# Performance work log

Measured on AMD Instinct MI355X. Metric: run time of the kernel, lower is better.

The kernel has to match this reference:

```python
import jax, jax.numpy as jnp
import numpy as np

EPS = 1e-6

def normalize(a):
    # L1 row-normalization over the last dim (works for [b,f,n,n] and [b,n,n])
    return a / (jnp.sum(jnp.abs(a), axis=-1, keepdims=True) + EPS)

def setup_inputs() -> dict:
    key = jax.random.key(0)
    ks = jax.random.split(key, 10)
    B, NC, F_, NE, R = 32, 62, 256, 512, 16
    s = 0.05
    return {
        "x": jax.random.normal(ks[0], (B, NC, F_), dtype=jnp.float32),
        "p": jax.random.normal(ks[1], (NC, NC), dtype=jnp.float32) * s,
        "bias": jnp.zeros((NC, F_), dtype=jnp.float32),
        "q_mat": jax.random.normal(ks[2], (F_, F_), dtype=jnp.float32) * s,
        "theta": jax.random.normal(ks[3], (F_, NC * F_), dtype=jnp.float32) * s,
        "codebook": jax.random.normal(ks[4], (NE, F_), dtype=jnp.float32) * s,
        "se_w1": jax.random.normal(ks[5], (F_, F_ // R), dtype=jnp.float32) * s,
        "se_b1": jnp.zeros((F_ // R,), dtype=jnp.float32),
        "se_w2": jax.random.normal(ks[6], (F_ // R, F_), dtype=jnp.float32) * s,
        "se_b2": jnp.zeros((F_,), dtype=jnp.float32),
    }

def reference(x, p, bias, q_mat, theta, codebook, se_w1, se_b1, se_w2, se_b2):
    elu = jax.nn.elu
    commitment = 0.25
    # o = p @ x + bias : [b, nc, f]
    o = jnp.einsum('ij,bjd->bid', p, x) + bias
    # g = ELU(o @ q @ theta) : [b, nc, nc*f]
    g = elu((o @ q_mat) @ theta)
    b, nc = g.shape[0], g.shape[1]
    adj = g.reshape(b, nc, nc, -1).transpose(0, 3, 1, 2)  # [b, f, nc, nc]
    adj = normalize(adj)
    # ---- VQ codebook quantization ----
    d = codebook.shape[1]
    z = adj.transpose(0, 2, 3, 1).reshape(-1, d)  # [b*nc*nc, d]
    dist = (jnp.sum(z * z, axis=-1, keepdims=True)
            - 2.0 * z @ codebook.T
            + jnp.sum(codebook * codebook, axis=-1))  # [N, num_embedding]
    idx = jnp.argmin(dist, axis=-1)
    zq = codebook[idx]
    e_loss = jnp.mean((jax.lax.stop_gradient(zq) - z) ** 2)
    q_loss = jnp.mean((zq - jax.lax.stop_gradient(z)) ** 2)
    vq_loss = q_loss + commitment * e_loss
    zq_st = z + jax.lax.stop_gradient(zq - z)  # straight-through
    counts = jnp.zeros((codebook.shape[0],), dtype=z.dtype).at[idx].add(1.0)
    probs = counts / idx.shape[0]
    usage = jnp.exp(-jnp.sum(probs * jnp.log(probs + 1e-10)))  # perplexity
    adj_recon = zq_st.reshape(b, nc, nc, d).transpose(0, 3, 1, 2)  # [b, f, nc, nc]
    # ---- SE block + residual ----
    s = jnp.mean(adj_recon, axis=(2, 3))  # squeeze: [b, f]
    s = jax.nn.sigmoid(jax.nn.relu(s @ se_w1 + se_b1) @ se_w2 + se_b2)
    adj_recon = elu(adj_recon * s[:, :, None, None] + adj_recon)
    # reduce over feature channels, ELU, normalize : [b, nc, nc]
    adj_recon = normalize(elu(jnp.sum(adj_recon, axis=1)))
    return (vq_loss, adj_recon, usage, codebook)
```

## Files before the change

kernel.cpp:

```cpp
#include <hip/hip_runtime.h>
#include <math.h>

#define B_   32
#define NCq  62
#define F_   256
#define NE   512
#define M_   (B_*NCq)
#define NCOL (NCq*F_)
#define NZ   (M_*NCq)
#define EPSF 1e-6f

typedef unsigned short ushort_t;
typedef unsigned int uint_t;
typedef _Float16 h8_t __attribute__((ext_vector_type(8)));
typedef float f4_t __attribute__((ext_vector_type(4)));

__device__ __forceinline__ float eluf(float x){ return x > 0.0f ? x : expm1f(x); }

__device__ __forceinline__ int sw64(int row, int piece){
    return row*64 + ((piece ^ (row&7))*8);
}
__device__ __forceinline__ void gl_lds(const _Float16* g, _Float16* l){
    __builtin_amdgcn_global_load_lds((const __attribute__((address_space(1))) void*)g,
                                     (__attribute__((address_space(3))) void*)l, 16, 0, 0);
}

__global__ __launch_bounds__(256) void k_split_th(const float* __restrict__ TH,
                                                  _Float16* __restrict__ THf){
    __shared__ float tile[32][33];
    int n0 = blockIdx.x * 32, k0 = blockIdx.y * 32;
    int tid = threadIdx.x;
    int cc = tid & 31, rr = tid >> 5;
    #pragma unroll
    for(int p=0;p<4;p++){
        int kk = rr + p*8;
        tile[kk][cc] = TH[(size_t)(k0+kk)*NCOL + n0 + cc];
    }
    __syncthreads();
    #pragma unroll
    for(int p=0;p<4;p++){
        int nn = rr + p*8;
        THf[(size_t)(n0+nn)*F_ + k0 + cc] = (_Float16)tile[cc][nn];
    }
}

__global__ __launch_bounds__(256) void k_prep(const float* __restrict__ cb,
                                              _Float16* __restrict__ CBf,
                                              float* __restrict__ cnorm, float* __restrict__ out_cb){
    int e = blockIdx.x; int d = threadIdx.x;
    float v = cb[e*F_ + d];
    out_cb[e*F_ + d] = v;
    CBf[e*F_ + d] = (_Float16)v;
    float s = v*v;
    #pragma unroll
    for(int m=32;m;m>>=1) s += __shfl_xor(s, m, 64);
    __shared__ float red[4];
    if((threadIdx.x & 63)==0) red[threadIdx.x>>6] = s;
    __syncthreads();
    if(threadIdx.x==0) cnorm[e] = red[0]+red[1]+red[2]+red[3];
}

__global__ __launch_bounds__(256) void k_ot(const float* __restrict__ x, const float* __restrict__ p,
                                            const float* __restrict__ bias, const float* __restrict__ q,
                                            _Float16* __restrict__ Tf){
    int bi = blockIdx.x; int d = threadIdx.x;
    int b = bi / NCq, i = bi % NCq;
    __shared__ float pr[NCq];
    __shared__ float orow[F_];
    if(d < NCq) pr[d] = p[i*NCq + d];
    __syncthreads();
    float acc = bias[i*F_ + d];
    const float* xb = x + (size_t)b*NCq*F_ + d;
    #pragma unroll 2
    for(int j=0;j<NCq;j++) acc = fmaf(pr[j], xb[j*F_], acc);
    orow[d] = acc;
    __syncthreads();
    float t = 0.f;
    #pragma unroll 4
    for(int k=0;k<F_;k++) t = fmaf(orow[k], q[k*F_ + d], t);
    Tf[bi*F_ + d] = (_Float16)t;
}

__global__ __launch_bounds__(256,2) void k_gemm_g(const _Float16* __restrict__ Tf,
                                                  const _Float16* __restrict__ THf,
                                                  _Float16* __restrict__ Gf){
    __shared__ _Float16 As[128*64], Bs[256*64];
    int tid = threadIdx.x;
    int l = tid & 63, w = tid >> 6;
    int wr = w >> 1, wc = w & 1;
    int m = l & 15, quad = l >> 4;
    int row0 = blockIdx.x * 128, col0 = blockIdx.y * 256;
    int wbase = tid & 192;
    f4_t acc[4][8] = {};
    for(int kc=0; kc<F_; kc+=64){
        #pragma unroll
        for(int p2=0;p2<4;p2++){
            int idx = p2*256 + tid;
            int row = idx >> 3, psw = idx & 7;
            int porig = psw ^ (row&7);
            int rclamp = row0 + row; if(rclamp >= M_) rclamp = M_-1;
            gl_lds(&Tf[(size_t)rclamp*F_ + kc + porig*8], &As[(p2*256 + wbase)*8]);
        }
        #pragma unroll
        for(int p2=0;p2<8;p2++){
            int idx = p2*256 + tid;
            int row = idx >> 3, psw = idx & 7;
            int porig = psw ^ (row&7);
            gl_lds(&THf[(size_t)(col0 + row)*F_ + kc + porig*8], &Bs[(p2*256 + wbase)*8]);
        }
        __syncthreads();
        #pragma unroll
        for(int ks=0;ks<2;ks++){
            h8_t a[4];
            #pragma unroll
            for(int mt=0;mt<4;mt++){
                int row = wr*64 + mt*16 + m;
                a[mt] = *(const h8_t*)&As[sw64(row, ks*4 + quad)];
            }
            #pragma unroll
            for(int nt=0;nt<8;nt++){
                int col = wc*128 + nt*16 + m;
                h8_t b = *(const h8_t*)&Bs[sw64(col, ks*4 + quad)];
                #pragma unroll
                for(int mt=0;mt<4;mt++)
                    acc[mt][nt] = __builtin_amdgcn_mfma_f32_16x16x32_f16(a[mt], b, acc[mt][nt], 0,0,0);
            }
        }
        __syncthreads();
    }
    #pragma unroll
    for(int mt=0;mt<4;mt++){
        #pragma unroll
        for(int nt=0;nt<8;nt++){
            int rowb = row0 + wr*64 + mt*16 + quad*4;
            int colb = col0 + wc*128 + nt*16 + m;
            #pragma unroll
            for(int r=0;r<4;r++){
                int row = rowb + r;
                if(row < M_) Gf[(size_t)row*NCOL + colb] = (_Float16)eluf(acc[mt][nt][r]);
            }
        }
    }
}

__global__ __launch_bounds__(256) void k_den(_Float16* __restrict__ Gf, double* __restrict__ loss_sum){
    int bi = blockIdx.x;
    int tid = threadIdx.x;
    int dg = tid & 31, jg = tid >> 5;
    __shared__ float l1[8][32][8];
    __shared__ float l2[8][32][8];
    __shared__ float invsh[32][8];
    float v[8][8];
    float a1[8] = {}, a2[8] = {};
    size_t base = (size_t)bi*NCOL + dg*8;
    #pragma unroll
    for(int p=0;p<8;p++){
        int j = jg + p*8;
        if(j < NCq){
            h8_t g = *(const h8_t*)&Gf[base + (size_t)j*F_];
            #pragma unroll
            for(int i=0;i<8;i++){
                float t = (float)g[i];
                v[p][i] = t;
                a1[i] += fabsf(t);
                a2[i] = fmaf(t, t, a2[i]);
            }
        }
    }
    #pragma unroll
    for(int i=0;i<8;i++){ l1[jg][dg][i] = a1[i]; l2[jg][dg][i] = a2[i]; }
    __syncthreads();
    if(jg == 0){
        float part = 0.f;
        #pragma unroll
        for(int i=0;i<8;i++){
            float s1 = 0.f, s2 = 0.f;
            #pragma unroll
            for(int q2=0;q2<8;q2++){ s1 += l1[q2][dg][i]; s2 += l2[q2][dg][i]; }
            float inv = 1.0f/(s1 + EPSF);
            invsh[dg][i] = inv;
            part += s2*inv*inv;
        }
        #pragma unroll
        for(int mk=16;mk;mk>>=1) part += __shfl_xor(part, mk, 32);
        if(tid == 0) atomicAdd(loss_sum, (double)part);
    }
    __syncthreads();
    float inv[8];
    #pragma unroll
    for(int i=0;i<8;i++) inv[i] = invsh[dg][i];
    #pragma unroll
    for(int p=0;p<8;p++){
        int j = jg + p*8;
        if(j < NCq){
            h8_t z;
            #pragma unroll
            for(int i=0;i<8;i++) z[i] = (_Float16)(v[p][i]*inv[i]);
            *(h8_t*)&Gf[base + (size_t)j*F_] = z;
        }
    }
}

__global__ __launch_bounds__(256,2) void k_vq(const _Float16* __restrict__ Zf,
                                              const _Float16* __restrict__ CBf,
                                              const float* __restrict__ cnorm,
                                              float* __restrict__ pmin, int* __restrict__ pidx){
    __shared__ _Float16 As[128*64], Bs[256*64];
    int tid = threadIdx.x;
    int l = tid & 63, w = tid >> 6;
    int wr = w >> 1, wc = w & 1;
    int m = l & 15, quad = l >> 4;
    int n_base = blockIdx.x * 128;
    int e0 = blockIdx.y * 256;
    int wbase = tid & 192;
    f4_t acc[4][8] = {};
    for(int kc=0; kc<F_; kc+=64){
        #pragma unroll
        for(int p2=0;p2<4;p2++){
            int idx = p2*256 + tid;
            int row = idx >> 3, psw = idx & 7;
            int porig = psw ^ (row&7);
            gl_lds(&Zf[(size_t)(n_base + row)*F_ + kc + porig*8], &As[(p2*256 + wbase)*8]);
        }
        #pragma unroll
        for(int p2=0;p2<8;p2++){
            int idx = p2*256 + tid;
            int row = idx >> 3, psw = idx & 7;
            int porig = psw ^ (row&7);
            gl_lds(&CBf[(size_t)(e0 + row)*F_ + kc + porig*8], &Bs[(p2*256 + wbase)*8]);
        }
        __syncthreads();
        #pragma unroll
        for(int ks=0;ks<2;ks++){
            h8_t a[4];
            #pragma unroll
            for(int mt=0;mt<4;mt++){
                int row = wr*64 + mt*16 + m;
                a[mt] = *(const h8_t*)&As[sw64(row, ks*4 + quad)];
            }
            #pragma unroll
            for(int nt=0;nt<8;nt++){
                int col = wc*128 + nt*16 + m;
                h8_t b = *(const h8_t*)&Bs[sw64(col, ks*4 + quad)];
                #pragma unroll
                for(int mt=0;mt<4;mt++)
                    acc[mt][nt] = __builtin_amdgcn_mfma_f32_16x16x32_f16(a[mt], b, acc[mt][nt], 0,0,0);
            }
        }
        __syncthreads();
    }
    #pragma unroll
    for(int mt=0;mt<4;mt++){
        float bv[4]; int bix[4];
        #pragma unroll
        for(int r=0;r<4;r++){ bv[r] = 3.4e38f; bix[r] = 0; }
        #pragma unroll
        for(int nt=0;nt<8;nt++){
            int e = e0 + wc*128 + nt*16 + m;
            float cn = cnorm[e];
            #pragma unroll
            for(int r=0;r<4;r++){
                float vv = cn - 2.0f*acc[mt][nt][r];
                if(vv < bv[r]){ bv[r] = vv; bix[r] = e; }
            }
        }
        #pragma unroll
        for(int r=0;r<4;r++){
            float vv = bv[r]; int ix = bix[r];
            #pragma unroll
            for(int mk=8;mk;mk>>=1){
                float ov = __shfl_xor(vv, mk, 64);
                int   oi = __shfl_xor(ix, mk, 64);
                if(ov < vv || (ov == vv && oi < ix)){ vv = ov; ix = oi; }
            }
            if(m == 0){
                int n = n_base + wr*64 + mt*16 + quad*4 + r;
                int slot = blockIdx.y*2 + wc;
                pmin[n*4 + slot] = vv;
                pidx[n*4 + slot] = ix;
            }
        }
    }
}

__global__ __launch_bounds__(1024) void k_fin(const float* __restrict__ pmin, const int* __restrict__ pidx,
                                              int* __restrict__ idx,
                                              int* __restrict__ counts, int* __restrict__ countb,
                                              double* __restrict__ loss_sum){
    int b = blockIdx.x;
    int t = threadIdx.x;
    __shared__ int hist[NE];
    __shared__ float red[16];
    #pragma unroll
    for(int e=t; e<NE; e+=1024) hist[e] = 0;
    __syncthreads();
    float msum = 0.f;
    int n0 = b * (NCq*NCq);
    for(int i=t; i<NCq*NCq; i+=1024){
        int n = n0 + i;
        float4 pv = *(const float4*)&pmin[n*4];
        int4   pi = *(const int4*)&pidx[n*4];
        float bv = pv.x; int bix = pi.x;
        if(pv.y < bv || (pv.y==bv && pi.y<bix)){ bv=pv.y; bix=pi.y; }
        if(pv.z < bv || (pv.z==bv && pi.z<bix)){ bv=pv.z; bix=pi.z; }
        if(pv.w < bv || (pv.w==bv && pi.w<bix)){ bv=pv.w; bix=pi.w; }
        idx[n] = bix;
        atomicAdd(&hist[bix], 1);
        msum += bv;
    }
    #pragma unroll
    for(int m=32;m;m>>=1) msum += __shfl_xor(msum, m, 64);
    if((t&63)==0) red[t>>6] = msum;
    __syncthreads();
    if(t==0){
        float s = 0.f;
        #pragma unroll
        for(int i2=0;i2<16;i2++) s += red[i2];
        atomicAdd(loss_sum, (double)s);
    }
    for(int e=t; e<NE; e+=1024){
        int c = hist[e];
        countb[b*NE + e] = c;
        if(c) atomicAdd(&counts[e], c);
    }
}

__global__ __launch_bounds__(256) void k_scal(const int* __restrict__ counts, const double* __restrict__ loss_sum,
                                              float* __restrict__ out){
    int t = threadIdx.x;
    float ent = 0.f;
    for(int e=t; e<NE; e+=256){
        float pr = (float)counts[e] / (float)NZ;
        ent += pr * logf(pr + 1e-10f);
    }
    #pragma unroll
    for(int m=32;m;m>>=1) ent += __shfl_xor(ent,m,64);
    __shared__ float red[4];
    if((t&63)==0) red[t>>6]=ent;
    __syncthreads();
    if(t==0){
        float e2 = red[0]+red[1]+red[2]+red[3];
        out[1+NZ] = expf(-e2);
        out[0] = (float)(1.25 * (*loss_sum) / ((double)NZ * (double)F_));
    }
}

__global__ __launch_bounds__(256) void k_se(const int* __restrict__ countb, const float* __restrict__ cb,
                                            const float* __restrict__ w1, const float* __restrict__ b1,
                                            const float* __restrict__ w2, const float* __restrict__ b2,
                                            float* __restrict__ s2p1){
    int b = blockIdx.x; int d = threadIdx.x;
    __shared__ float cnt[NE];
    __shared__ float s_sh[F_];
    __shared__ float h_sh[16];
    cnt[d]       = (float)countb[b*NE + d];
    cnt[d + 256] = (float)countb[b*NE + d + 256];
    __syncthreads();
    float s = 0.f;
    for(int e=0;e<NE;e++) s = fmaf(cnt[e], cb[e*F_ + d], s);
    s *= (1.0f/(float)(NCq*NCq));
    s_sh[d] = s;
    __syncthreads();
    if(d < 16){
        float h = b1[d];
        for(int k=0;k<F_;k++) h = fmaf(s_sh[k], w1[k*16 + d], h);
        h_sh[d] = fmaxf(h, 0.f);
    }
    __syncthreads();
    float v = b2[d];
    #pragma unroll
    for(int r=0;r<16;r++) v = fmaf(h_sh[r], w2[r*F_ + d], v);
    s2p1[b*F_ + d] = 1.0f + 1.0f/(1.0f + expf(-v));
}

__global__ __launch_bounds__(256) void k_w(const float* __restrict__ cb, const float* __restrict__ s2p1,
                                           float* __restrict__ wtab){
    int b = blockIdx.x; int eg = blockIdx.y;
    int wv = threadIdx.x>>6, lane = threadIdx.x&63;
    __shared__ float m_sh[F_];
    m_sh[threadIdx.x] = s2p1[b*F_ + threadIdx.x];
    __syncthreads();
    int e = eg*4 + wv;
    float4 c4 = *(const float4*)&cb[e*F_ + lane*4];
    float s = eluf(c4.x*m_sh[lane*4]) + eluf(c4.y*m_sh[lane*4+1])
            + eluf(c4.z*m_sh[lane*4+2]) + eluf(c4.w*m_sh[lane*4+3]);
    #pragma unroll
    for(int m2=32;m2;m2>>=1) s += __shfl_xor(s,m2,64);
    if(lane==0) wtab[b*NE + e] = s;
}

__global__ __launch_bounds__(64) void k_out(const int* __restrict__ idx, const float* __restrict__ wtab,
                                            float* __restrict__ out){
    int bi = blockIdx.x; int j = threadIdx.x;
    int b = bi / NCq;
    float v = 0.f;
    if(j < NCq) v = eluf(wtab[b*NE + idx[bi*NCq + j]]);
    float a = fabsf(v);
    #pragma unroll
    for(int m=32;m;m>>=1) a += __shfl_xor(a,m,64);
    if(j < NCq) out[1 + bi*NCq + j] = v / (a + EPSF);
}

extern "C" void kernel_launch(void* const* d_in, const int* in_sizes, int n_in,
                              void* d_out, int out_size, void* d_ws, size_t ws_size,
                              hipStream_t stream){
    (void)in_sizes; (void)n_in; (void)out_size; (void)ws_size;
    const float* x    = (const float*)d_in[0];
    const float* p    = (const float*)d_in[1];
    const float* bias = (const float*)d_in[2];
    const float* q    = (const float*)d_in[3];
    const float* th   = (const float*)d_in[4];
    const float* cb   = (const float*)d_in[5];
    const float* w1   = (const float*)d_in[6];
    const float* b1   = (const float*)d_in[7];
    const float* w2   = (const float*)d_in[8];
    const float* b2   = (const float*)d_in[9];
    float* out = (float*)d_out;
    char* ws = (char*)d_ws;
    size_t off = 0;
    auto alloc = [&](size_t bytes){ void* ptr = ws + off; off = (off + bytes + 255) & ~255ull; return ptr; };
    _Float16* Gf   = (_Float16*)alloc((size_t)NZ*F_*sizeof(_Float16));
    _Float16* THf  = (_Float16*)alloc((size_t)F_*NCOL*sizeof(_Float16));
    _Float16* Tf   = (_Float16*)alloc((size_t)M_*F_*sizeof(_Float16));
    _Float16* CBf  = (_Float16*)alloc((size_t)NE*F_*sizeof(_Float16));
    float*    CN   = (float*)   alloc((size_t)NE*sizeof(float));
    float*    PMIN = (float*)   alloc((size_t)NZ*4*sizeof(float));
    int*      PIDX = (int*)     alloc((size_t)NZ*4*sizeof(int));
    int*      IDX  = (int*)     alloc((size_t)NZ*sizeof(int));
    char*     zbase= (char*)    alloc(8 + NE*sizeof(int));
    double*   LOSS   = (double*)zbase;
    int*      COUNTS = (int*)(zbase + 8);
    int*      COUNTB = (int*)   alloc((size_t)B_*NE*sizeof(int));
    float*    S2P1 = (float*)alloc((size_t)B_*F_*sizeof(float));
    float*    WTAB = (float*)alloc((size_t)B_*NE*sizeof(float));

    (void)hipMemsetAsync(zbase, 0, 8 + NE*sizeof(int), stream);
    dim3 gth(NCOL/32, F_/32);
    k_split_th<<<gth, 256, 0, stream>>>(th, THf);
    k_prep<<<NE, 256, 0, stream>>>(cb, CBf, CN, out + 1 + NZ + 1);
    k_ot<<<M_, 256, 0, stream>>>(x, p, bias, q, Tf);
    dim3 g3((M_ + 127)/128, NCOL/256);
    k_gemm_g<<<g3, 256, 0, stream>>>(Tf, THf, Gf);
    k_den<<<M_, 256, 0, stream>>>(Gf, LOSS);
    dim3 g5(NZ/128, 2);
    k_vq<<<g5, 256, 0, stream>>>(Gf, CBf, CN, PMIN, PIDX);
    k_fin<<<B_, 1024, 0, stream>>>(PMIN, PIDX, IDX, COUNTS, COUNTB, LOSS);
    k_scal<<<1, 256, 0, stream>>>(COUNTS, LOSS, out);
    k_se<<<B_, 256, 0, stream>>>(COUNTB, cb, w1, b1, w2, b2, S2P1);
    dim3 g8(B_, NE/4);
    k_w<<<g8, 256, 0, stream>>>(cb, S2P1, WTAB);
    k_out<<<M_, 64, 0, stream>>>(IDX, WTAB, out);
}
```

Baseline: 303.1 us.

## Double-buffer LDS tiles with K=32 stages in both MFMA GEMM kernels

Both GEMM kernels (the theta projection and the VQ distance GEMM) now split K into eight 32-wide stages held in two ping-pong LDS buffers. The global-to-LDS load for the next stage is issued before the MFMAs on the current stage, with a single barrier per stage and a new 4-piece XOR swizzle. The aim is to overlap global memory latency with compute and drop one barrier per iteration. Launch bounds are raised to 3 blocks per CU, which tightens the register budget for the 128-float accumulator and could cause spilling.

Measured after the change: 349.5 us. 15.3% more time.

```diff
diff --git a/kernel.cpp b/kernel.cpp
--- a/kernel.cpp
+++ b/kernel.cpp
@@ -17,8 +17,8 @@
 
 __device__ __forceinline__ float eluf(float x){ return x > 0.0f ? x : expm1f(x); }
 
-__device__ __forceinline__ int sw64(int row, int piece){
-    return row*64 + ((piece ^ (row&7))*8);
+__device__ __forceinline__ int sw_off(int row, int piece){
+    return row*32 + ((piece ^ ((row>>1)&3))*8);
 }
 __device__ __forceinline__ void gl_lds(const _Float16* g, _Float16* l){
     __builtin_amdgcn_global_load_lds((const __attribute__((address_space(1))) void*)g,
@@ -81,10 +81,10 @@
     Tf[bi*F_ + d] = (_Float16)t;
 }
 
-__global__ __launch_bounds__(256,2) void k_gemm_g(const _Float16* __restrict__ Tf,
+__global__ __launch_bounds__(256,3) void k_gemm_g(const _Float16* __restrict__ Tf,
                                                   const _Float16* __restrict__ THf,
                                                   _Float16* __restrict__ Gf){
-    __shared__ _Float16 As[128*64], Bs[256*64];
+    __shared__ _Float16 As[2][128*32], Bs[2][256*32];
     int tid = threadIdx.x;
     int l = tid & 63, w = tid >> 6;
     int wr = w >> 1, wc = w & 1;
@@ -92,41 +92,44 @@
     int row0 = blockIdx.x * 128, col0 = blockIdx.y * 256;
     int wbase = tid & 192;
     f4_t acc[4][8] = {};
-    for(int kc=0; kc<F_; kc+=64){
+    auto stage = [&](int kc, int buf){
+        #pragma unroll
+        for(int p2=0;p2<2;p2++){
+            int idx = p2*256 + tid;
+            int row = idx >> 2, psw = idx & 3;
+            int porig = psw ^ ((row>>1)&3);
+            int rclamp = row0 + row; if(rclamp >= M_) rclamp = M_-1;
+            gl_lds(&Tf[(size_t)rclamp*F_ + kc + porig*8], &As[buf][(p2*256 + wbase)*8]);
+        }
         #pragma unroll
         for(int p2=0;p2<4;p2++){
             int idx = p2*256 + tid;
-            int row = idx >> 3, psw = idx & 7;
-            int porig = psw ^ (row&7);
-            int rclamp = row0 + row; if(rclamp >= M_) rclamp = M_-1;
-            gl_lds(&Tf[(size_t)rclamp*F_ + kc + porig*8], &As[(p2*256 + wbase)*8]);
-        }
-        #pragma unroll
-        for(int p2=0;p2<8;p2++){
-            int idx = p2*256 + tid;
-            int row = idx >> 3, psw = idx & 7;
-            int porig = psw ^ (row&7);
-            gl_lds(&THf[(size_t)(col0 + row)*F_ + kc + porig*8], &Bs[(p2*256 + wbase)*8]);
-        }
+            int row = idx >> 2, psw = idx & 3;
+            int porig = psw ^ ((row>>1)&3);
+            gl_lds(&THf[(size_t)(col0 + row)*F_ + kc + porig*8], &Bs[buf][(p2*256 + wbase)*8]);
+        }
+    };
+    stage(0, 0);
+    #pragma unroll
+    for(int i=0;i<8;i++){
         __syncthreads();
-        #pragma unroll
-        for(int ks=0;ks<2;ks++){
-            h8_t a[4];
-            #pragma unroll
-            for(int mt=0;mt<4;mt++){
-                int row = wr*64 + mt*16 + m;
-                a[mt] = *(const h8_t*)&As[sw64(row, ks*4 + quad)];
-            }
-            #pragma unroll
-            for(int nt=0;nt<8;nt++){
-                int col = wc*128 + nt*16 + m;
-                h8_t b = *(const h8_t*)&Bs[sw64(col, ks*4 + quad)];
-                #pragma unroll
-                for(int mt=0;mt<4;mt++)
-                    acc[mt][nt] = __builtin_amdgcn_mfma_f32_16x16x32_f16(a[mt], b, acc[mt][nt], 0,0,0);
-            }
-        }
-        __syncthreads();
+        if(i < 7) stage((i+1)*32, (i+1)&1);
+        const _Float16* Ab = As[i&1];
+        const _Float16* Bb = Bs[i&1];
+        h8_t a[4];
+        #pragma unroll
+        for(int mt=0;mt<4;mt++){
+            int row = wr*64 + mt*16 + m;
+            a[mt] = *(const h8_t*)&Ab[sw_off(row, quad)];
+        }
+        #pragma unroll
+        for(int nt=0;nt<8;nt++){
+            int col = wc*128 + nt*16 + m;
+            h8_t b = *(const h8_t*)&Bb[sw_off(col, quad)];
+            #pragma unroll
+            for(int mt=0;mt<4;mt++)
+                acc[mt][nt] = __builtin_amdgcn_mfma_f32_16x16x32_f16(a[mt], b, acc[mt][nt], 0,0,0);
+        }
     }
     #pragma unroll
     for(int mt=0;mt<4;mt++){
@@ -201,11 +204,11 @@
     }
 }
 
-__global__ __launch_bounds__(256,2) void k_vq(const _Float16* __restrict__ Zf,
+__global__ __launch_bounds__(256,3) void k_vq(const _Float16* __restrict__ Zf,
                                               const _Float16* __restrict__ CBf,
                                               const float* __restrict__ cnorm,
                                               float* __restrict__ pmin, int* __restrict__ pidx){
-    __shared__ _Float16 As[128*64], Bs[256*64];
+    __shared__ _Float16 As[2][128*32], Bs[2][256*32];
     int tid = threadIdx.x;
     int l = tid & 63, w = tid >> 6;
     int wr = w >> 1, wc = w & 1;
@@ -214,40 +217,43 @@
     int e0 = blockIdx.y * 256;
     int wbase = tid & 192;
     f4_t acc[4][8] = {};
-    for(int kc=0; kc<F_; kc+=64){
+    auto stage = [&](int kc, int buf){
+        #pragma unroll
+        for(int p2=0;p2<2;p2++){
+            int idx = p2*256 + tid;
+            int row = idx >> 2, psw = idx & 3;
+            int porig = psw ^ ((row>>1)&3);
+            gl_lds(&Zf[(size_t)(n_base + row)*F_ + kc + porig*8], &As[buf][(p2*256 + wbase)*8]);
+        }
         #pragma unroll
         for(int p2=0;p2<4;p2++){
             int idx = p2*256 + tid;
-            int row = idx >> 3, psw = idx & 7;
-            int porig = psw ^ (row&7);
-            gl_lds(&Zf[(size_t)(n_base + row)*F_ + kc + porig*8], &As[(p2*256 + wbase)*8]);
-        }
-        #pragma unroll
-        for(int p2=0;p2<8;p2++){
-            int idx = p2*256 + tid;
-            int row = idx >> 3, psw = idx & 7;
-            int porig = psw ^ (row&7);
-            gl_lds(&CBf[(size_t)(e0 + row)*F_ + kc + porig*8], &Bs[(p2*256 + wbase)*8]);
-        }
+            int row = idx >> 2, psw = idx & 3;
+            int porig = psw ^ ((row>>1)&3);
+            gl_lds(&CBf[(size_t)(e0 + row)*F_ + kc + porig*8], &Bs[buf][(p2*256 + wbase)*8]);
+        }
+    };
+    stage(0, 0);
+    #pragma unroll
+    for(int i=0;i<8;i++){
         __syncthreads();
-        #pragma unroll
-        for(int ks=0;ks<2;ks++){
-            h8_t a[4];
-            #pragma unroll
-            for(int mt=0;mt<4;mt++){
-                int row = wr*64 + mt*16 + m;
-                a[mt] = *(const h8_t*)&As[sw64(row, ks*4 + quad)];
-            }
-            #pragma unroll
-            for(int nt=0;nt<8;nt++){
-                int col = wc*128 + nt*16 + m;
-                h8_t b = *(const h8_t*)&Bs[sw64(col, ks*4 + quad)];
-                #pragma unroll
-                for(int mt=0;mt<4;mt++)
-                    acc[mt][nt] = __builtin_amdgcn_mfma_f32_16x16x32_f16(a[mt], b, acc[mt][nt], 0,0,0);
-            }
-        }
-        __syncthreads();
+        if(i < 7) stage((i+1)*32, (i+1)&1);
+        const _Float16* Ab = As[i&1];
+        const _Float16* Bb = Bs[i&1];
+        h8_t a[4];
+        #pragma unroll
+        for(int mt=0;mt<4;mt++){
+            int row = wr*64 + mt*16 + m;
+            a[mt] = *(const h8_t*)&Ab[sw_off(row, quad)];
+        }
+        #pragma unroll
+        for(int nt=0;nt<8;nt++){
+            int col = wc*128 + nt*16 + m;
+            h8_t b = *(const h8_t*)&Bb[sw_off(col, quad)];
+            #pragma unroll
+            for(int mt=0;mt<4;mt++)
+                acc[mt][nt] = __builtin_amdgcn_mfma_f32_16x16x32_f16(a[mt], b, acc[mt][nt], 0,0,0);
+        }
     }
     #pragma unroll
     for(int mt=0;mt<4;mt++){
```

## Fuse prologue and epilogue kernels, replace atomics with per-block partial sums

Applied to the files above, without the earlier changes.

Merges the theta transpose, codebook prep and o@q kernels into one launch that dispatches on block index. Merges the finalize, SE, weight-table and output kernels into a single per-batch kernel. Replaces double atomics and the memset with per-block float partials that one scalar kernel reduces. This cuts launch count and serialization gaps between small kernels. In exchange the fused post kernel runs on only 32 blocks, and the loss is now summed in float rather than double.

New measurement: 299.0 us. About the same (-1.3%).

```diff
diff --git a/kernel.cpp b/kernel.cpp
--- a/kernel.cpp
+++ b/kernel.cpp
@@ -10,8 +10,6 @@
 #define NZ   (M_*NCq)
 #define EPSF 1e-6f
 
-typedef unsigned short ushort_t;
-typedef unsigned int uint_t;
 typedef _Float16 h8_t __attribute__((ext_vector_type(8)));
 typedef float f4_t __attribute__((ext_vector_type(4)));
 
@@ -25,60 +23,62 @@
                                      (__attribute__((address_space(3))) void*)l, 16, 0, 0);
 }
 
-__global__ __launch_bounds__(256) void k_split_th(const float* __restrict__ TH,
-                                                  _Float16* __restrict__ THf){
-    __shared__ float tile[32][33];
-    int n0 = blockIdx.x * 32, k0 = blockIdx.y * 32;
+#define NB_SPLIT (496*8)
+#define NB_PREP  NE
+#define NB_OT    M_
+__global__ __launch_bounds__(256) void k_pre(const float* __restrict__ TH, _Float16* __restrict__ THf,
+                                             const float* __restrict__ cb, _Float16* __restrict__ CBf,
+                                             float* __restrict__ cnorm, float* __restrict__ out_cb,
+                                             const float* __restrict__ x, const float* __restrict__ p,
+                                             const float* __restrict__ bias, const float* __restrict__ q,
+                                             _Float16* __restrict__ Tf){
+    int bid = blockIdx.x;
     int tid = threadIdx.x;
-    int cc = tid & 31, rr = tid >> 5;
-    #pragma unroll
-    for(int p=0;p<4;p++){
-        int kk = rr + p*8;
-        tile[kk][cc] = TH[(size_t)(k0+kk)*NCOL + n0 + cc];
-    }
-    __syncthreads();
-    #pragma unroll
-    for(int p=0;p<4;p++){
-        int nn = rr + p*8;
-        THf[(size_t)(n0+nn)*F_ + k0 + cc] = (_Float16)tile[cc][nn];
-    }
-}
-
-__global__ __launch_bounds__(256) void k_prep(const float* __restrict__ cb,
-                                              _Float16* __restrict__ CBf,
-                                              float* __restrict__ cnorm, float* __restrict__ out_cb){
-    int e = blockIdx.x; int d = threadIdx.x;
-    float v = cb[e*F_ + d];
-    out_cb[e*F_ + d] = v;
-    CBf[e*F_ + d] = (_Float16)v;
-    float s = v*v;
-    #pragma unroll
-    for(int m=32;m;m>>=1) s += __shfl_xor(s, m, 64);
-    __shared__ float red[4];
-    if((threadIdx.x & 63)==0) red[threadIdx.x>>6] = s;
-    __syncthreads();
-    if(threadIdx.x==0) cnorm[e] = red[0]+red[1]+red[2]+red[3];
-}
-
-__global__ __launch_bounds__(256) void k_ot(const float* __restrict__ x, const float* __restrict__ p,
-                                            const float* __restrict__ bias, const float* __restrict__ q,
-                                            _Float16* __restrict__ Tf){
-    int bi = blockIdx.x; int d = threadIdx.x;
-    int b = bi / NCq, i = bi % NCq;
-    __shared__ float pr[NCq];
-    __shared__ float orow[F_];
-    if(d < NCq) pr[d] = p[i*NCq + d];
-    __syncthreads();
-    float acc = bias[i*F_ + d];
-    const float* xb = x + (size_t)b*NCq*F_ + d;
-    #pragma unroll 2
-    for(int j=0;j<NCq;j++) acc = fmaf(pr[j], xb[j*F_], acc);
-    orow[d] = acc;
-    __syncthreads();
-    float t = 0.f;
-    #pragma unroll 4
-    for(int k=0;k<F_;k++) t = fmaf(orow[k], q[k*F_ + d], t);
-    Tf[bi*F_ + d] = (_Float16)t;
+    if(bid < NB_SPLIT){
+        __shared__ float tile[32][33];
+        int n0 = (bid % 496) * 32, k0 = (bid / 496) * 32;
+        int cc = tid & 31, rr = tid >> 5;
+        #pragma unroll
+        for(int pp=0;pp<4;pp++){
+            int kk = rr + pp*8;
+            tile[kk][cc] = TH[(size_t)(k0+kk)*NCOL + n0 + cc];
+        }
+        __syncthreads();
+        #pragma unroll
+        for(int pp=0;pp<4;pp++){
+            int nn = rr + pp*8;
+            THf[(size_t)(n0+nn)*F_ + k0 + cc] = (_Float16)tile[cc][nn];
+        }
+    } else if(bid < NB_SPLIT + NB_PREP){
+        int e = bid - NB_SPLIT; int d = tid;
+        float v = cb[e*F_ + d];
+        out_cb[e*F_ + d] = v;
+        CBf[e*F_ + d] = (_Float16)v;
+        float s = v*v;
+        #pragma unroll
+        for(int m=32;m;m>>=1) s += __shfl_xor(s, m, 64);
+        __shared__ float red[4];
+        if((tid & 63)==0) red[tid>>6] = s;
+        __syncthreads();
+        if(tid==0) cnorm[e] = red[0]+red[1]+red[2]+red[3];
+    } else {
+        int bi = bid - NB_SPLIT - NB_PREP; int d = tid;
+        int b = bi / NCq, i = bi % NCq;
+        __shared__ float pr[NCq];
+        __shared__ float orow[F_];
+        if(d < NCq) pr[d] = p[i*NCq + d];
+        __syncthreads();
+        float acc = bias[i*F_ + d];
+        const float* xb = x + (size_t)b*NCq*F_ + d;
+        #pragma unroll 2
+        for(int j=0;j<NCq;j++) acc = fmaf(pr[j], xb[j*F_], acc);
+        orow[d] = acc;
+        __syncthreads();
+        float t = 0.f;
+        #pragma unroll 4
+        for(int k=0;k<F_;k++) t = fmaf(orow[k], q[k*F_ + d], t);
+        Tf[bi*F_ + d] = (_Float16)t;
+    }
 }
 
 __global__ __launch_bounds__(256,2) void k_gemm_g(const _Float16* __restrict__ Tf,
@@ -143,7 +143,7 @@
     }
 }
 
-__global__ __launch_bounds__(256) void k_den(_Float16* __restrict__ Gf, double* __restrict__ loss_sum){
+__global__ __launch_bounds__(256) void k_den(_Float16* __restrict__ Gf, float* __restrict__ lp){
     int bi = blockIdx.x;
     int tid = threadIdx.x;
     int dg = tid & 31, jg = tid >> 5;
@@ -183,7 +183,7 @@
         }
         #pragma unroll
         for(int mk=16;mk;mk>>=1) part += __shfl_xor(part, mk, 32);
-        if(tid == 0) atomicAdd(loss_sum, (double)part);
+        if(tid == 0) lp[bi] = part;
     }
     __syncthreads();
     float inv[8];
@@ -283,15 +283,22 @@
     }
 }
 
-__global__ __launch_bounds__(1024) void k_fin(const float* __restrict__ pmin, const int* __restrict__ pidx,
-                                              int* __restrict__ idx,
-                                              int* __restrict__ counts, int* __restrict__ countb,
-                                              double* __restrict__ loss_sum){
+__global__ __launch_bounds__(1024) void k_post(const float* __restrict__ pmin, const int* __restrict__ pidx,
+                                               int* __restrict__ idx, int* __restrict__ countb,
+                                               float* __restrict__ lossb,
+                                               const float* __restrict__ cb,
+                                               const float* __restrict__ w1, const float* __restrict__ b1,
+                                               const float* __restrict__ w2, const float* __restrict__ b2,
+                                               float* __restrict__ out){
     int b = blockIdx.x;
     int t = threadIdx.x;
     __shared__ int hist[NE];
     __shared__ float red[16];
-    #pragma unroll
+    __shared__ float sp[4][F_];
+    __shared__ float s_sh[F_];
+    __shared__ float h_sh[16];
+    __shared__ float s2p1[F_];
+    __shared__ float wt[NE];
     for(int e=t; e<NE; e+=1024) hist[e] = 0;
     __syncthreads();
     float msum = 0.f;
@@ -316,89 +323,83 @@
         float s = 0.f;
         #pragma unroll
         for(int i2=0;i2<16;i2++) s += red[i2];
-        atomicAdd(loss_sum, (double)s);
-    }
-    for(int e=t; e<NE; e+=1024){
-        int c = hist[e];
-        countb[b*NE + e] = c;
-        if(c) atomicAdd(&counts[e], c);
-    }
-}
-
-__global__ __launch_bounds__(256) void k_scal(const int* __restrict__ counts, const double* __restrict__ loss_sum,
+        lossb[b] = s;
+    }
+    for(int e=t; e<NE; e+=1024) countb[b*NE + e] = hist[e];
+    {
+        int d = t & 255, qq = t >> 8;
+        float s = 0.f;
+        for(int e=qq*128; e<(qq+1)*128; e++) s = fmaf((float)hist[e], cb[e*F_ + d], s);
+        sp[qq][d] = s;
+    }
+    __syncthreads();
+    if(t < F_) s_sh[t] = (sp[0][t]+sp[1][t]+sp[2][t]+sp[3][t]) * (1.0f/(float)(NCq*NCq));
+    __syncthreads();
+    if(t < 16){
+        float h = b1[t];
+        for(int k=0;k<F_;k++) h = fmaf(s_sh[k], w1[k*16 + t], h);
+        h_sh[t] = fmaxf(h, 0.f);
+    }
+    __syncthreads();
+    if(t < F_){
+        float v = b2[t];
+        #pragma unroll
+        for(int r=0;r<16;r++) v = fmaf(h_sh[r], w2[r*F_ + t], v);
+        s2p1[t] = 1.0f + 1.0f/(1.0f + expf(-v));
+    }
+    __syncthreads();
+    {
+        int wv = t >> 6, lane = t & 63;
+        for(int e = wv; e < NE; e += 16){
+            float4 c4 = *(const float4*)&cb[e*F_ + lane*4];
+            float s = eluf(c4.x*s2p1[lane*4]) + eluf(c4.y*s2p1[lane*4+1])
+                    + eluf(c4.z*s2p1[lane*4+2]) + eluf(c4.w*s2p1[lane*4+3]);
+            #pragma unroll
+            for(int m2=32;m2;m2>>=1) s += __shfl_xor(s, m2, 64);
+            if(lane==0) wt[e] = s;
+        }
+    }
+    __syncthreads();
+    {
+        int wv = t >> 6, lane = t & 63;
+        for(int i = wv; i < NCq; i += 16){
+            int bi = b*NCq + i;
+            float v = 0.f;
+            if(lane < NCq) v = eluf(wt[idx[bi*NCq + lane]]);
+            float a = fabsf(v);
+            #pragma unroll
+            for(int m2=32;m2;m2>>=1) a += __shfl_xor(a, m2, 64);
+            if(lane < NCq) out[1 + bi*NCq + lane] = v / (a + EPSF);
+        }
+    }
+}
+
+__global__ __launch_bounds__(256) void k_scal(const int* __restrict__ countb,
+                                              const float* __restrict__ lp, const float* __restrict__ lossb,
                                               float* __restrict__ out){
     int t = threadIdx.x;
     float ent = 0.f;
     for(int e=t; e<NE; e+=256){
-        float pr = (float)counts[e] / (float)NZ;
+        int c = 0;
+        #pragma unroll 4
+        for(int b=0;b<B_;b++) c += countb[b*NE + e];
+        float pr = (float)c / (float)NZ;
         ent += pr * logf(pr + 1e-10f);
     }
-    #pragma unroll
-    for(int m=32;m;m>>=1) ent += __shfl_xor(ent,m,64);
-    __shared__ float red[4];
-    if((t&63)==0) red[t>>6]=ent;
+    float ls = 0.f;
+    for(int i=t; i<M_; i+=256) ls += lp[i];
+    if(t < B_) ls += lossb[t];
+    #pragma unroll
+    for(int m=32;m;m>>=1){ ent += __shfl_xor(ent,m,64); ls += __shfl_xor(ls,m,64); }
+    __shared__ float red[4], red2[4];
+    if((t&63)==0){ red[t>>6]=ent; red2[t>>6]=ls; }
     __syncthreads();
     if(t==0){
         float e2 = red[0]+red[1]+red[2]+red[3];
+        float l2 = red2[0]+red2[1]+red2[2]+red2[3];
         out[1+NZ] = expf(-e2);
-        out[0] = (float)(1.25 * (*loss_sum) / ((double)NZ * (double)F_));
-    }
-}
-
-__global__ __launch_bounds__(256) void k_se(const int* __restrict__ countb, const float* __restrict__ cb,
-                                            const float* __restrict__ w1, const float* __restrict__ b1,
-                                            const float* __restrict__ w2, const float* __restrict__ b2,
-                                            float* __restrict__ s2p1){
-    int b = blockIdx.x; int d = threadIdx.x;
-    __shared__ float cnt[NE];
-    __shared__ float s_sh[F_];
-    __shared__ float h_sh[16];
-    cnt[d]       = (float)countb[b*NE + d];
-    cnt[d + 256] = (float)countb[b*NE + d + 256];
-    __syncthreads();
-    float s = 0.f;
-    for(int e=0;e<NE;e++) s = fmaf(cnt[e], cb[e*F_ + d], s);
-    s *= (1.0f/(float)(NCq*NCq));
-    s_sh[d] = s;
-    __syncthreads();
-    if(d < 16){
-        float h = b1[d];
-        for(int k=0;k<F_;k++) h = fmaf(s_sh[k], w1[k*16 + d], h);
-        h_sh[d] = fmaxf(h, 0.f);
-    }
-    __syncthreads();
-    float v = b2[d];
-    #pragma unroll
-    for(int r=0;r<16;r++) v = fmaf(h_sh[r], w2[r*F_ + d], v);
-    s2p1[b*F_ + d] = 1.0f + 1.0f/(1.0f + expf(-v));
-}
-
-__global__ __launch_bounds__(256) void k_w(const float* __restrict__ cb, const float* __restrict__ s2p1,
-                                           float* __restrict__ wtab){
-    int b = blockIdx.x; int eg = blockIdx.y;
-    int wv = threadIdx.x>>6, lane = threadIdx.x&63;
-    __shared__ float m_sh[F_];
-    m_sh[threadIdx.x] = s2p1[b*F_ + threadIdx.x];
-    __syncthreads();
-    int e = eg*4 + wv;
-    float4 c4 = *(const float4*)&cb[e*F_ + lane*4];
-    float s = eluf(c4.x*m_sh[lane*4]) + eluf(c4.y*m_sh[lane*4+1])
-            + eluf(c4.z*m_sh[lane*4+2]) + eluf(c4.w*m_sh[lane*4+3]);
-    #pragma unroll
-    for(int m2=32;m2;m2>>=1) s += __shfl_xor(s,m2,64);
-    if(lane==0) wtab[b*NE + e] = s;
-}
-
-__global__ __launch_bounds__(64) void k_out(const int* __restrict__ idx, const float* __restrict__ wtab,
-                                            float* __restrict__ out){
-    int bi = blockIdx.x; int j = threadIdx.x;
-    int b = bi / NCq;
-    float v = 0.f;
-    if(j < NCq) v = eluf(wtab[b*NE + idx[bi*NCq + j]]);
-    float a = fabsf(v);
-    #pragma unroll
-    for(int m=32;m;m>>=1) a += __shfl_xor(a,m,64);
-    if(j < NCq) out[1 + bi*NCq + j] = v / (a + EPSF);
+        out[0] = (float)(1.25 * (double)l2 / ((double)NZ * (double)F_));
+    }
 }
 
 extern "C" void kernel_launch(void* const* d_in, const int* in_sizes, int n_in,
@@ -427,27 +428,17 @@
     float*    PMIN = (float*)   alloc((size_t)NZ*4*sizeof(float));
     int*      PIDX = (int*)     alloc((size_t)NZ*4*sizeof(int));
     int*      IDX  = (int*)     alloc((size_t)NZ*sizeof(int));
-    char*     zbase= (char*)    alloc(8 + NE*sizeof(int));
-    double*   LOSS   = (double*)zbase;
-    int*      COUNTS = (int*)(zbase + 8);
-    int*      COUNTB = (int*)   alloc((size_t)B_*NE*sizeof(int));
-    float*    S2P1 = (float*)alloc((size_t)B_*F_*sizeof(float));
-    float*    WTAB = (float*)alloc((size_t)B_*NE*sizeof(float));
-
-    (void)hipMemsetAsync(zbase, 0, 8 + NE*sizeof(int), stream);
-    dim3 gth(NCOL/32, F_/32);
-    k_split_th<<<gth, 256, 0, stream>>>(th, THf);
-    k_prep<<<NE, 256, 0, stream>>>(cb, CBf, CN, out + 1 + NZ + 1);
-    k_ot<<<M_, 256, 0, stream>>>(x, p, bias, q, Tf);
+    float*    LP    = (float*)  alloc((size_t)M_*sizeof(float));
+    float*    LOSSB = (float*)  alloc((size_t)B_*sizeof(float));
+    int*      COUNTB= (int*)    alloc((size_t)B_*NE*sizeof(int));
+
+    k_pre<<<NB_SPLIT + NB_PREP + NB_OT, 256, 0, stream>>>(th, THf, cb, CBf, CN, out + 1 + NZ + 1,
+                                                          x, p, bias, q, Tf);
     dim3 g3((M_ + 127)/128, NCOL/256);
     k_gemm_g<<<g3, 256, 0, stream>>>(Tf, THf, Gf);
-    k_den<<<M_, 256, 0, stream>>>(Gf, LOSS);
+    k_den<<<M_, 256, 0, stream>>>(Gf, LP);
     dim3 g5(NZ/128, 2);
     k_vq<<<g5, 256, 0, stream>>>(Gf, CBf, CN, PMIN, PIDX);
-    k_fin<<<B_, 1024, 0, stream>>>(PMIN, PIDX, IDX, COUNTS, COUNTB, LOSS);
-    k_scal<<<1, 256, 0, stream>>>(COUNTS, LOSS, out);
-    k_se<<<B_, 256, 0, stream>>>(COUNTB, cb, w1, b1, w2, b2, S2P1);
-    dim3 g8(B_, NE/4);
-    k_w<<<g8, 256, 0, stream>>>(cb, S2P1, WTAB);
-    k_out<<<M_, 64, 0, stream>>>(IDX, WTAB, out);
-}
+    k_post<<<B_, 1024, 0, stream>>>(PMIN, PIDX, IDX, COUNTB, LOSSB, cb, w1, b1, w2, b2, out);
+    k_scal<<<1, 256, 0, stream>>>(COUNTB, LP, LOSSB, out);
+}
```
